# Kernel optimization log

Measured on AMD Instinct MI355X. Metric: run time of the kernel, lower is better.

## Reference

```python
import jax, jax.numpy as jnp
import numpy as np

N_HEADS = 12
LN_EPS = 1e-5


def _layernorm(x, g, b):
    mu = jnp.mean(x, axis=-1, keepdims=True)
    var = jnp.var(x, axis=-1, keepdims=True)
    return (x - mu) * jax.lax.rsqrt(var + LN_EPS) * g + b


def setup_inputs() -> dict:
    key = jax.random.key(0)
    ks = jax.random.split(key, 16)
    L, V, D, F, MAXS = 4, 32000, 768, 3072, 2048
    B, S = 2, 1024
    sd = 0.02
    inp = {
        'x': jax.random.randint(ks[0], (B, S), 0, V, dtype=jnp.int64),
        'tok_emb': jax.random.normal(ks[1], (V, D), jnp.float32) * sd,
        'pos_emb': jax.random.normal(ks[2], (MAXS, D), jnp.float32) * sd,
        'Wq': jax.random.normal(ks[3], (L, D, D), jnp.float32) * sd,
        'bq': jnp.zeros((L, D), jnp.float32),
        'Wk': jax.random.normal(ks[4], (L, D, D), jnp.float32) * sd,
        'bk': jnp.zeros((L, D), jnp.float32),
        'Wv': jax.random.normal(ks[5], (L, D, D), jnp.float32) * sd,
        'bv': jnp.zeros((L, D), jnp.float32),
        'Wo': jax.random.normal(ks[6], (L, D, D), jnp.float32) * sd,
        'bo': jnp.zeros((L, D), jnp.float32),
        'W1': jax.random.normal(ks[7], (L, F, D), jnp.float32) * sd,
        'b1': jnp.zeros((L, F), jnp.float32),
        'W2': jax.random.normal(ks[8], (L, D, F), jnp.float32) * sd,
        'b2': jnp.zeros((L, D), jnp.float32),
        'ln1_g': jnp.ones((L, D), jnp.float32),
        'ln1_b': jnp.zeros((L, D), jnp.float32),
        'ln2_g': jnp.ones((L, D), jnp.float32),
        'ln2_b': jnp.zeros((L, D), jnp.float32),
        'lnf_g': jnp.ones((D,), jnp.float32),
        'lnf_b': jnp.zeros((D,), jnp.float32),
    }
    return inp


def reference(x, tok_emb, pos_emb, Wq, bq, Wk, bk, Wv, bv, Wo, bo,
              W1, b1, W2, b2, ln1_g, ln1_b, ln2_g, ln2_b, lnf_g, lnf_b):
    B, S = x.shape
    D = tok_emb.shape[1]
    L = Wq.shape[0]
    H = N_HEADS
    dk = D // H
    scale = 1.0 / jnp.sqrt(jnp.float32(dk))

    h = tok_emb[x] + pos_emb[:S][None]  # [B,S,D]  (dropout p=0 -> identity)
    causal = jnp.tril(jnp.ones((S, S), bool))  # [S,S]

    def split_heads(t):  # [B,S,D] -> [B,H,S,dk]
        return t.reshape(B, S, H, dk).transpose(0, 2, 1, 3)

    for l in range(L):
        y = _layernorm(h, ln1_g[l], ln1_b[l])
        q = split_heads(y @ Wq[l].T + bq[l])
        k = split_heads(y @ Wk[l].T + bk[l])
        v = split_heads(y @ Wv[l].T + bv[l])
        scores = jnp.einsum('bhqd,bhkd->bhqk', q, k) * scale
        scores = jnp.where(causal, scores, -jnp.inf)
        attn = jax.nn.softmax(scores, axis=-1)
        ctx = jnp.einsum('bhqk,bhkd->bhqd', attn, v)
        ctx = ctx.transpose(0, 2, 1, 3).reshape(B, S, D)
        h = h + (ctx @ Wo[l].T + bo[l])
        y2 = _layernorm(h, ln2_g[l], ln2_b[l])
        ff = jax.nn.relu(y2 @ W1[l].T + b1[l]) @ W2[l].T + b2[l]
        h = h + ff

    h = _layernorm(h, lnf_g, lnf_b)
    logits = h @ tok_emb.T  # tied LM head, no bias
    return logits
```

## Files before the change

### kernel.cpp

```cpp
#include <hip/hip_runtime.h>
#include <hip/hip_bf16.h>

typedef __bf16 bf16_t;
typedef __bf16 bf16x8 __attribute__((ext_vector_type(8)));
typedef float floatx4 __attribute__((ext_vector_type(4)));

#define D_MODEL 768
#define N_HEADS 12
#define DK 64
#define SEQ 1024
#define BATCH 2
#define NROWS (BATCH * SEQ)
#define FFN 3072
#define VOCAB 32000
#define N_LAYERS 4
#define LN_EPS 1e-5f

__device__ __forceinline__ float block_reduce_256(float v, bool is_max, float* sb) {
#pragma unroll
    for (int off = 32; off > 0; off >>= 1) {
        float o = __shfl_down(v, off, 64);
        v = is_max ? fmaxf(v, o) : (v + o);
    }
    int lane = threadIdx.x & 63, wid = threadIdx.x >> 6;
    if (lane == 0) sb[wid] = v;
    __syncthreads();
    float r = is_max ? fmaxf(fmaxf(sb[0], sb[1]), fmaxf(sb[2], sb[3]))
                     : (sb[0] + sb[1]) + (sb[2] + sb[3]);
    __syncthreads();
    return r;
}

__global__ __launch_bounds__(256) void embed_kernel(const int* __restrict__ x,
                                                    const float* __restrict__ tok,
                                                    const float* __restrict__ pos,
                                                    float* __restrict__ h) {
    int row = blockIdx.x;
    int s = row & (SEQ - 1);
    int t = x[row];
    const float* te = tok + (size_t)t * D_MODEL;
    const float* pe = pos + (size_t)s * D_MODEL;
    float* out = h + (size_t)row * D_MODEL;
    int tid = threadIdx.x;
    out[tid]       = te[tid]       + pe[tid];
    out[tid + 256] = te[tid + 256] + pe[tid + 256];
    out[tid + 512] = te[tid + 512] + pe[tid + 512];
}

__global__ __launch_bounds__(256) void cvt_bf16_kernel(const float* __restrict__ src,
                                                       bf16_t* __restrict__ dst) {
    size_t i = ((size_t)blockIdx.x * 256 + threadIdx.x) * 8;
    const float4 a = *(const float4*)(src + i);
    const float4 b = *(const float4*)(src + i + 4);
    bf16x8 o;
    o[0] = (bf16_t)a.x; o[1] = (bf16_t)a.y; o[2] = (bf16_t)a.z; o[3] = (bf16_t)a.w;
    o[4] = (bf16_t)b.x; o[5] = (bf16_t)b.y; o[6] = (bf16_t)b.z; o[7] = (bf16_t)b.w;
    *(bf16x8*)(dst + i) = o;
}
static_assert((VOCAB * D_MODEL) % 2048 == 0, "cvt tiling");
static_assert((N_LAYERS * D_MODEL * D_MODEL) % 2048 == 0, "cvt tiling");
static_assert((N_LAYERS * FFN * D_MODEL) % 2048 == 0, "cvt tiling");

__global__ __launch_bounds__(256) void pack_qkvw_kernel(const float* __restrict__ Wq,
                                                        const float* __restrict__ Wk,
                                                        const float* __restrict__ Wv,
                                                        bf16_t* __restrict__ dst) {
    size_t e = ((size_t)blockIdx.x * 256 + threadIdx.x) * 8;
    const int PER_L = 3 * D_MODEL * D_MODEL;
    const int SEG   = D_MODEL * D_MODEL;
    int l   = (int)(e / PER_L);
    int rem = (int)(e - (size_t)l * PER_L);
    int n   = rem / D_MODEL;
    int c   = rem - n * D_MODEL;
    int seg = n / D_MODEL;
    int sr  = n - seg * D_MODEL;
    const float* src = (seg == 0 ? Wq : seg == 1 ? Wk : Wv) +
                       (size_t)l * SEG + (size_t)sr * D_MODEL + c;
    const float4 a = *(const float4*)src;
    const float4 b = *(const float4*)(src + 4);
    bf16x8 o;
    o[0] = (bf16_t)a.x; o[1] = (bf16_t)a.y; o[2] = (bf16_t)a.z; o[3] = (bf16_t)a.w;
    o[4] = (bf16_t)b.x; o[5] = (bf16_t)b.y; o[6] = (bf16_t)b.z; o[7] = (bf16_t)b.w;
    *(bf16x8*)(dst + e) = o;
}

__global__ __launch_bounds__(256) void pack_bias_kernel(const float* __restrict__ bq,
                                                        const float* __restrict__ bk,
                                                        const float* __restrict__ bv,
                                                        float* __restrict__ dst) {
    int i = blockIdx.x * 256 + threadIdx.x;
    int l = i / (3 * D_MODEL);
    int n = i - l * (3 * D_MODEL);
    int seg = n / D_MODEL;
    int sr  = n - seg * D_MODEL;
    dst[i] = (seg == 0 ? bq : seg == 1 ? bk : bv)[l * D_MODEL + sr];
}

__global__ __launch_bounds__(256) void ln_kernel(const float* __restrict__ h,
                                                 const float* __restrict__ g,
                                                 const float* __restrict__ b,
                                                 bf16_t* __restrict__ y) {
    __shared__ float sb[4];
    int row = blockIdx.x;
    const float* xr = h + (size_t)row * D_MODEL;
    int t = threadIdx.x;
    float v0 = xr[t], v1 = xr[t + 256], v2 = xr[t + 512];
    float s  = block_reduce_256(v0 + v1 + v2, false, sb);
    float s2 = block_reduce_256(v0 * v0 + v1 * v1 + v2 * v2, false, sb);
    float mu  = s * (1.0f / D_MODEL);
    float var = s2 * (1.0f / D_MODEL) - mu * mu;
    float inv = rsqrtf(var + LN_EPS);
    bf16_t* yr = y + (size_t)row * D_MODEL;
    yr[t]       = (bf16_t)((v0 - mu) * inv * g[t]       + b[t]);
    yr[t + 256] = (bf16_t)((v1 - mu) * inv * g[t + 256] + b[t + 256]);
    yr[t + 512] = (bf16_t)((v2 - mu) * inv * g[t + 512] + b[t + 512]);
}

template <typename OutT, bool RELU, bool HAS_BIAS, bool HAS_RES, bool MSWAP>
__global__ __launch_bounds__(256) void gemm_bt(const bf16_t* __restrict__ A,
                                               const float* __restrict__ W,
                                               const float* __restrict__ bias,
                                               const float* __restrict__ res,
                                               OutT* __restrict__ C,
                                               int M, int N, int K) {
    const int LDR = 40;
    __shared__ bf16_t As[64 * LDR];
    __shared__ bf16_t Bs[64 * LDR];
    const int m0 = (MSWAP ? blockIdx.x : blockIdx.y) * 64;
    const int n0 = (MSWAP ? blockIdx.y : blockIdx.x) * 64;
    const int tid  = threadIdx.x;
    const int wave = tid >> 6;
    const int lane = tid & 63;
    const int q    = lane >> 4;
    const int ln16 = lane & 15;

    floatx4 acc[4] = {{0.f, 0.f, 0.f, 0.f}, {0.f, 0.f, 0.f, 0.f},
                      {0.f, 0.f, 0.f, 0.f}, {0.f, 0.f, 0.f, 0.f}};

    const int srow = tid >> 2;
    const int scol = (tid & 3) * 8;
    const bf16_t* Aptr = A + (size_t)(m0 + srow) * K + scol;
    const float*  Wptr = W + (size_t)(n0 + srow) * K + scol;

    for (int k0 = 0; k0 < K; k0 += 32) {
        *(uint4*)(&As[srow * LDR + scol]) = *(const uint4*)(Aptr + k0);
        float4 w0 = *(const float4*)(Wptr + k0);
        float4 w1 = *(const float4*)(Wptr + k0 + 4);
        bf16x8 wb;
        wb[0] = (bf16_t)w0.x; wb[1] = (bf16_t)w0.y; wb[2] = (bf16_t)w0.z; wb[3] = (bf16_t)w0.w;
        wb[4] = (bf16_t)w1.x; wb[5] = (bf16_t)w1.y; wb[6] = (bf16_t)w1.z; wb[7] = (bf16_t)w1.w;
        *(bf16x8*)(&Bs[srow * LDR + scol]) = wb;
        __syncthreads();
        const bf16x8 a = *(const bf16x8*)(&As[(wave * 16 + ln16) * LDR + q * 8]);
#pragma unroll
        for (int nt = 0; nt < 4; nt++) {
            const bf16x8 b = *(const bf16x8*)(&Bs[(nt * 16 + ln16) * LDR + q * 8]);
            acc[nt] = __builtin_amdgcn_mfma_f32_16x16x32_bf16(a, b, acc[nt], 0, 0, 0);
        }
        __syncthreads();
    }

#pragma unroll
    for (int nt = 0; nt < 4; nt++) {
        const int n = n0 + nt * 16 + ln16;
        float bv = 0.f;
        if constexpr (HAS_BIAS) bv = bias[n];
#pragma unroll
        for (int r = 0; r < 4; r++) {
            const int m = m0 + wave * 16 + q * 4 + r;
            float v = acc[nt][r] + bv;
            if constexpr (RELU) v = fmaxf(v, 0.f);
            if constexpr (HAS_RES) v += res[(size_t)m * N + n];
            C[(size_t)m * N + n] = (OutT)v;
        }
    }
}

typedef __attribute__((address_space(3))) unsigned int lds_uint;
typedef const __attribute__((address_space(1))) unsigned int glb_uint;
__device__ __forceinline__ void gload16(const bf16_t* g, bf16_t* l) {
    __builtin_amdgcn_global_load_lds((glb_uint*)g, (lds_uint*)l, 16, 0, 0);
}

template <typename OutT, bool RELU, bool HAS_BIAS, bool HAS_RES, bool NTS, int TN>
__global__ __launch_bounds__(256) void gemm128(const bf16_t* __restrict__ A,
                                               const bf16_t* __restrict__ W,
                                               const float* __restrict__ bias,
                                               const float* __restrict__ res,
                                               OutT* __restrict__ C,
                                               int M, int N, int K) {
    constexpr int NFR = TN / 32;
    __shared__ __align__(16) bf16_t As[128 * 32];
    __shared__ __align__(16) bf16_t Bs[TN * 32];
    const int m0 = blockIdx.x * 128;
    const int n0 = blockIdx.y * TN;
    const int tid  = threadIdx.x;
    const int wave = tid >> 6;
    const int lane = tid & 63;
    const int q    = lane >> 4;
    const int ln16 = lane & 15;
    const int wr   = wave >> 1;
    const int wc   = wave & 1;

    floatx4 acc[4][NFR];
#pragma unroll
    for (int i = 0; i < 4; i++)
#pragma unroll
        for (int j = 0; j < NFR; j++) acc[i][j] = (floatx4){0.f, 0.f, 0.f, 0.f};

    const int srow = lane >> 2;
    const int scol = (lane & 3) * 8;
    const bf16_t* Ag = A + (size_t)(m0 + wave * 32 + srow) * K + scol;
    const bf16_t* Wg = W + (size_t)(n0 + wave * (TN / 4) + srow) * K + scol;
    bf16_t* As0 = &As[wave * 1024];
    bf16_t* Bs0 = &Bs[wave * (TN / 4) * 32];

    for (int k0 = 0; k0 < K; k0 += 32) {
        gload16(Ag + k0, As0);
        gload16(Ag + (size_t)16 * K + k0, As0 + 512);
        gload16(Wg + k0, Bs0);
        if constexpr (TN == 128) gload16(Wg + (size_t)16 * K + k0, Bs0 + 512);
        __syncthreads();
        bf16x8 af[4], bfg[NFR];
#pragma unroll
        for (int mt = 0; mt < 4; mt++)
            af[mt] = *(const bf16x8*)&As[(wr * 64 + mt * 16 + ln16) * 32 + q * 8];
#pragma unroll
        for (int nt = 0; nt < NFR; nt++)
            bfg[nt] = *(const bf16x8*)&Bs[(wc * (TN / 2) + nt * 16 + ln16) * 32 + q * 8];
#pragma unroll
        for (int mt = 0; mt < 4; mt++)
#pragma unroll
            for (int nt = 0; nt < NFR; nt++)
                acc[mt][nt] = __builtin_amdgcn_mfma_f32_16x16x32_bf16(af[mt], bfg[nt], acc[mt][nt], 0, 0, 0);
        __syncthreads();
    }

#pragma unroll
    for (int mt = 0; mt < 4; mt++)
#pragma unroll
        for (int nt = 0; nt < NFR; nt++) {
            const int n = n0 + wc * (TN / 2) + nt * 16 + ln16;
            float bv = 0.f;
            if constexpr (HAS_BIAS) bv = bias[n];
#pragma unroll
            for (int r = 0; r < 4; r++) {
                const int m = m0 + wr * 64 + mt * 16 + q * 4 + r;
                float v = acc[mt][nt][r] + bv;
                if constexpr (RELU) v = fmaxf(v, 0.f);
                if constexpr (HAS_RES) v += res[(size_t)m * N + n];
                if constexpr (NTS) {
                    __builtin_nontemporal_store((OutT)v, &C[(size_t)m * N + n]);
                } else {
                    C[(size_t)m * N + n] = (OutT)v;
                }
            }
        }
}

__global__ __launch_bounds__(256) void attn_kernel(const bf16_t* __restrict__ Q,
                                                   const bf16_t* __restrict__ K,
                                                   const bf16_t* __restrict__ V,
                                                   bf16_t* __restrict__ ctx,
                                                   int ld) {
    __shared__ bf16_t smem[12288];
    bf16_t* Qs  = smem;
    bf16_t* Ks  = smem + 4096;
    bf16_t* Vts = smem + 8192;
    bf16_t* Ps  = smem;

    const int qt  = blockIdx.x;
    const int bh  = blockIdx.y;
    const int b   = bh / N_HEADS;
    const int hh  = bh - b * N_HEADS;
    const int tid  = threadIdx.x;
    const int wave = tid >> 6;
    const int lane = tid & 63;
    const int quad = lane >> 4;
    const int ln16 = lane & 15;
    const int q0   = qt * 64;
    const size_t base = (size_t)(b * SEQ) * ld + hh * DK;

    const int r0 = tid >> 3;
    const int cg = tid & 7;

    {
        const bf16_t* src = Q + base + (size_t)q0 * ld;
        *(uint4*)&Qs[r0 * 64 + cg * 8]        = *(const uint4*)(src + (size_t)r0 * ld + cg * 8);
        *(uint4*)&Qs[(r0 + 32) * 64 + cg * 8] = *(const uint4*)(src + (size_t)(r0 + 32) * ld + cg * 8);
    }
    __syncthreads();
    const bf16x8 aq0 = *(const bf16x8*)&Qs[(wave * 16 + ln16) * 64 + quad * 8];
    const bf16x8 aq1 = *(const bf16x8*)&Qs[(wave * 16 + ln16) * 64 + 32 + quad * 8];

    float m_run[4] = {-1e30f, -1e30f, -1e30f, -1e30f};
    float l_run[4] = {0.f, 0.f, 0.f, 0.f};
    floatx4 o[4] = {{0.f, 0.f, 0.f, 0.f}, {0.f, 0.f, 0.f, 0.f},
                    {0.f, 0.f, 0.f, 0.f}, {0.f, 0.f, 0.f, 0.f}};
    const float scale = 0.125f;

    for (int j0 = 0; j0 <= q0; j0 += 64) {
        __syncthreads();
        const bf16_t* ksrc = K + base + (size_t)j0 * ld;
        const bf16_t* vsrc = V + base + (size_t)j0 * ld;
#pragma unroll
        for (int half = 0; half < 2; half++) {
            const int j = r0 + half * 32;
            *(uint4*)&Ks[j * 64 + cg * 8] = *(const uint4*)(ksrc + (size_t)j * ld + cg * 8);
            const bf16x8 vv = *(const bf16x8*)(vsrc + (size_t)j * ld + cg * 8);
#pragma unroll
            for (int i = 0; i < 8; i++) {
                const int d = cg * 8 + i;
                Vts[d * 64 + (((j >> 3) ^ cg) << 3) + (j & 7)] = vv[i];
            }
        }
        __syncthreads();

        floatx4 s[4];
#pragma unroll
        for (int nt = 0; nt < 4; nt++) {
            const bf16x8 bk0 = *(const bf16x8*)&Ks[(nt * 16 + ln16) * 64 + quad * 8];
            const bf16x8 bk1 = *(const bf16x8*)&Ks[(nt * 16 + ln16) * 64 + 32 + quad * 8];
            floatx4 z = {0.f, 0.f, 0.f, 0.f};
            z = __builtin_amdgcn_mfma_f32_16x16x32_bf16(aq0, bk0, z, 0, 0, 0);
            z = __builtin_amdgcn_mfma_f32_16x16x32_bf16(aq1, bk1, z, 0, 0, 0);
            s[nt] = z;
        }
        const bool diag = (j0 == q0);
#pragma unroll
        for (int nt = 0; nt < 4; nt++)
#pragma unroll
            for (int r = 0; r < 4; r++) {
                float v = s[nt][r] * scale;
                if (diag && (nt * 16 + ln16 > wave * 16 + quad * 4 + r)) v = -1e30f;
                s[nt][r] = v;
            }

        float alpha[4];
#pragma unroll
        for (int r = 0; r < 4; r++) {
            float v = fmaxf(fmaxf(s[0][r], s[1][r]), fmaxf(s[2][r], s[3][r]));
#pragma unroll
            for (int off = 1; off < 16; off <<= 1) v = fmaxf(v, __shfl_xor(v, off, 64));
            const float m_new = fmaxf(m_run[r], v);
            alpha[r] = __expf(m_run[r] - m_new);
            m_run[r] = m_new;
        }
        float rsum[4] = {0.f, 0.f, 0.f, 0.f};
#pragma unroll
        for (int nt = 0; nt < 4; nt++)
#pragma unroll
            for (int r = 0; r < 4; r++) {
                const float p = __expf(s[nt][r] - m_run[r]);
                s[nt][r] = p;
                rsum[r] += p;
            }
#pragma unroll
        for (int r = 0; r < 4; r++) {
            float v = rsum[r];
#pragma unroll
            for (int off = 1; off < 16; off <<= 1) v += __shfl_xor(v, off, 64);
            l_run[r] = l_run[r] * alpha[r] + v;
        }
#pragma unroll
        for (int nt = 0; nt < 4; nt++)
#pragma unroll
            for (int r = 0; r < 4; r++) o[nt][r] *= alpha[r];

        bf16_t* Pw = Ps + wave * 1024;
#pragma unroll
        for (int nt = 0; nt < 4; nt++)
#pragma unroll
            for (int r = 0; r < 4; r++) {
                const int rr = quad * 4 + r;
                Pw[rr * 64 + (((nt * 2 + (ln16 >> 3)) ^ (rr & 7)) << 3) + (ln16 & 7)] = (bf16_t)s[nt][r];
            }
        const bf16x8 ap0 = *(const bf16x8*)&Pw[ln16 * 64 + ((quad ^ (ln16 & 7)) << 3)];
        const bf16x8 ap1 = *(const bf16x8*)&Pw[ln16 * 64 + (((quad + 4) ^ (ln16 & 7)) << 3)];

#pragma unroll
        for (int nt = 0; nt < 4; nt++) {
            const int d  = nt * 16 + ln16;
            const int dd = (nt * 2 + (ln16 >> 3)) & 7;
            const bf16x8 bv0 = *(const bf16x8*)&Vts[d * 64 + ((quad ^ dd) << 3)];
            const bf16x8 bv1 = *(const bf16x8*)&Vts[d * 64 + (((quad + 4) ^ dd) << 3)];
            o[nt] = __builtin_amdgcn_mfma_f32_16x16x32_bf16(ap0, bv0, o[nt], 0, 0, 0);
            o[nt] = __builtin_amdgcn_mfma_f32_16x16x32_bf16(ap1, bv1, o[nt], 0, 0, 0);
        }
    }

#pragma unroll
    for (int r = 0; r < 4; r++) {
        const float inv = 1.0f / l_run[r];
        const int m = q0 + wave * 16 + quad * 4 + r;
#pragma unroll
        for (int nt = 0; nt < 4; nt++) {
            ctx[(size_t)(b * SEQ + m) * D_MODEL + hh * DK + nt * 16 + ln16] = (bf16_t)(o[nt][r] * inv);
        }
    }
}

extern "C" void kernel_launch(void* const* d_in, const int* in_sizes, int n_in,
                              void* d_out, int out_size, void* d_ws, size_t ws_size,
                              hipStream_t stream) {
    const int*   x    = (const int*)d_in[0];
    const float* tok  = (const float*)d_in[1];
    const float* pos  = (const float*)d_in[2];
    const float* Wq   = (const float*)d_in[3];
    const float* bq   = (const float*)d_in[4];
    const float* Wk   = (const float*)d_in[5];
    const float* bk   = (const float*)d_in[6];
    const float* Wv   = (const float*)d_in[7];
    const float* bv   = (const float*)d_in[8];
    const float* Wo   = (const float*)d_in[9];
    const float* bo   = (const float*)d_in[10];
    const float* W1   = (const float*)d_in[11];
    const float* b1   = (const float*)d_in[12];
    const float* W2   = (const float*)d_in[13];
    const float* b2   = (const float*)d_in[14];
    const float* ln1g = (const float*)d_in[15];
    const float* ln1b = (const float*)d_in[16];
    const float* ln2g = (const float*)d_in[17];
    const float* ln2b = (const float*)d_in[18];
    const float* lnfg = (const float*)d_in[19];
    const float* lnfb = (const float*)d_in[20];

    char* ws = (char*)d_ws;
    const size_t OFF_H    = 0;
    const size_t OFF_Y    = 6291456;
    const size_t OFF_QKV  = 9437184;
    const size_t OFF_CTX  = 18874368;
    const size_t OFF_FF   = OFF_QKV;
    const size_t OFF_TOKB = 22020096;
    const size_t OFF_WB   = 71172096;
    const size_t OFF_BQKV = 127795200;
    const size_t END_ALL  = 127832064;
    const size_t END_TOKB = OFF_WB;

    const bool big_ws  = ws_size >= END_TOKB;
    const bool big2_ws = ws_size >= END_ALL;

    float*  h    = (float*)(ws + OFF_H);
    bf16_t* y    = (bf16_t*)(ws + OFF_Y);
    bf16_t* qkv  = (bf16_t*)(ws + OFF_QKV);
    bf16_t* qb   = qkv;
    bf16_t* kb   = qkv + 2048 * 768;
    bf16_t* vbuf = qkv + 2 * 2048 * 768;
    bf16_t* ctx  = (bf16_t*)(ws + OFF_CTX);
    bf16_t* ff   = (bf16_t*)(ws + OFF_FF);
    bf16_t* tokb = (bf16_t*)(ws + OFF_TOKB);
    bf16_t* wb   = (bf16_t*)(ws + OFF_WB);
    bf16_t* wqkvb = wb;
    bf16_t* wob   = wb + 7077888;
    bf16_t* w1b   = wb + 9437184;
    bf16_t* w2b   = wb + 18874368;
    float*  bqkv  = (float*)(ws + OFF_BQKV);
    float*  outp  = (float*)d_out;

    embed_kernel<<<NROWS, 256, 0, stream>>>(x, tok, pos, h);

    if (big_ws) {
        cvt_bf16_kernel<<<(VOCAB * D_MODEL) / 2048, 256, 0, stream>>>(tok, tokb);
    }
    if (big2_ws) {
        pack_qkvw_kernel<<<(N_LAYERS * 3 * D_MODEL * D_MODEL) / 2048, 256, 0, stream>>>(Wq, Wk, Wv, wqkvb);
        cvt_bf16_kernel<<<(N_LAYERS * D_MODEL * D_MODEL) / 2048, 256, 0, stream>>>(Wo, wob);
        cvt_bf16_kernel<<<(N_LAYERS * FFN * D_MODEL) / 2048, 256, 0, stream>>>(W1, w1b);
        cvt_bf16_kernel<<<(N_LAYERS * FFN * D_MODEL) / 2048, 256, 0, stream>>>(W2, w2b);
        pack_bias_kernel<<<(N_LAYERS * 3 * D_MODEL) / 256, 256, 0, stream>>>(bq, bk, bv, bqkv);
    }

    const dim3 g768(D_MODEL / 64, NROWS / 64);
    const dim3 gffn(FFN / 64, NROWS / 64);
    const dim3 gattn(SEQ / 64, BATCH * N_HEADS);

    for (int l = 0; l < N_LAYERS; l++) {
        const float* Wq_l = Wq + (size_t)l * D_MODEL * D_MODEL;
        const float* Wk_l = Wk + (size_t)l * D_MODEL * D_MODEL;
        const float* Wv_l = Wv + (size_t)l * D_MODEL * D_MODEL;
        const float* Wo_l = Wo + (size_t)l * D_MODEL * D_MODEL;
        const float* W1_l = W1 + (size_t)l * FFN * D_MODEL;
        const float* W2_l = W2 + (size_t)l * D_MODEL * FFN;

        ln_kernel<<<NROWS, 256, 0, stream>>>(h, ln1g + l * D_MODEL, ln1b + l * D_MODEL, y);

        if (big2_ws) {
            gemm128<bf16_t, false, true, false, false, 128>
                <<<dim3(NROWS / 128, (3 * D_MODEL) / 128), 256, 0, stream>>>(
                y, wqkvb + (size_t)l * 3 * D_MODEL * D_MODEL, bqkv + l * 3 * D_MODEL,
                nullptr, qkv, NROWS, 3 * D_MODEL, D_MODEL);

            attn_kernel<<<gattn, 256, 0, stream>>>(qkv, qkv + D_MODEL, qkv + 2 * D_MODEL, ctx, 3 * D_MODEL);

            gemm128<float, false, true, true, false, 64>
                <<<dim3(NROWS / 128, D_MODEL / 64), 256, 0, stream>>>(
                ctx, wob + (size_t)l * D_MODEL * D_MODEL, bo + l * D_MODEL,
                h, h, NROWS, D_MODEL, D_MODEL);

            ln_kernel<<<NROWS, 256, 0, stream>>>(h, ln2g + l * D_MODEL, ln2b + l * D_MODEL, y);

            gemm128<bf16_t, true, true, false, false, 128>
                <<<dim3(NROWS / 128, FFN / 128), 256, 0, stream>>>(
                y, w1b + (size_t)l * FFN * D_MODEL, b1 + l * FFN,
                nullptr, ff, NROWS, FFN, D_MODEL);

            gemm128<float, false, true, true, false, 64>
                <<<dim3(NROWS / 128, D_MODEL / 64), 256, 0, stream>>>(
                ff, w2b + (size_t)l * D_MODEL * FFN, b2 + l * D_MODEL,
                h, h, NROWS, D_MODEL, FFN);
        } else {
            gemm_bt<bf16_t, false, true, false, false><<<g768, 256, 0, stream>>>(
                y, Wq_l, bq + l * D_MODEL, nullptr, qb, NROWS, D_MODEL, D_MODEL);
            gemm_bt<bf16_t, false, true, false, false><<<g768, 256, 0, stream>>>(
                y, Wk_l, bk + l * D_MODEL, nullptr, kb, NROWS, D_MODEL, D_MODEL);
            gemm_bt<bf16_t, false, true, false, false><<<g768, 256, 0, stream>>>(
                y, Wv_l, bv + l * D_MODEL, nullptr, vbuf, NROWS, D_MODEL, D_MODEL);

            attn_kernel<<<gattn, 256, 0, stream>>>(qb, kb, vbuf, ctx, D_MODEL);

            gemm_bt<float, false, true, true, false><<<g768, 256, 0, stream>>>(
                ctx, Wo_l, bo + l * D_MODEL, h, h, NROWS, D_MODEL, D_MODEL);

            ln_kernel<<<NROWS, 256, 0, stream>>>(h, ln2g + l * D_MODEL, ln2b + l * D_MODEL, y);

            gemm_bt<bf16_t, true, true, false, false><<<gffn, 256, 0, stream>>>(
                y, W1_l, b1 + l * FFN, nullptr, ff, NROWS, FFN, D_MODEL);

            gemm_bt<float, false, true, true, false><<<g768, 256, 0, stream>>>(
                ff, W2_l, b2 + l * D_MODEL, h, h, NROWS, D_MODEL, FFN);
        }
    }

    ln_kernel<<<NROWS, 256, 0, stream>>>(h, lnfg, lnfb, y);

    if (big_ws) {
        gemm128<float, false, false, false, true, 128>
            <<<dim3(NROWS / 128, VOCAB / 128), 256, 0, stream>>>(
            y, tokb, nullptr, nullptr, outp, NROWS, VOCAB, D_MODEL);
    } else {
        gemm_bt<float, false, false, false, true><<<dim3(NROWS / 64, VOCAB / 64), 256, 0, stream>>>(
            y, tok, nullptr, nullptr, outp, NROWS, VOCAB, D_MODEL);
    }
}
```

Measured before the change: 1.255 ms.

## Deepen GEMM K-tile to 64 with XOR-swizzled LDS and XCD-aware block remap

The 128xTN GEMM now stages 64-wide K slices per iteration instead of 32, halving the number of barrier pairs per K loop and issuing two MFMA k-steps per sync. LDS rows are written and read with an XOR swizzle on the 16-byte chunk index to avoid bank conflicts at the new 128-byte row stride. A template flag optionally remaps block IDs so consecutive blocks are spread across the 8 XCDs for better L2 locality, and it replaces the nontemporal-store option. The cost is doubled LDS use, which may lower occupancy, and the last-layer logits output no longer uses nontemporal stores.

```diff
diff --git a/kernel.cpp b/kernel.cpp
--- a/kernel.cpp
+++ b/kernel.cpp
@@ -182,7 +182,7 @@
     __builtin_amdgcn_global_load_lds((glb_uint*)g, (lds_uint*)l, 16, 0, 0);
 }
 
-template <typename OutT, bool RELU, bool HAS_BIAS, bool HAS_RES, bool NTS, int TN>
+template <typename OutT, bool RELU, bool HAS_BIAS, bool HAS_RES, bool XSWZ, int TN>
 __global__ __launch_bounds__(256) void gemm128(const bf16_t* __restrict__ A,
                                                const bf16_t* __restrict__ W,
                                                const float* __restrict__ bias,
@@ -190,10 +190,22 @@
                                                OutT* __restrict__ C,
                                                int M, int N, int K) {
     constexpr int NFR = TN / 32;
-    __shared__ __align__(16) bf16_t As[128 * 32];
-    __shared__ __align__(16) bf16_t Bs[TN * 32];
-    const int m0 = blockIdx.x * 128;
-    const int n0 = blockIdx.y * TN;
+    __shared__ __align__(16) bf16_t As[128 * 64];
+    __shared__ __align__(16) bf16_t Bs[TN * 64];
+
+    int mb, nb;
+    if constexpr (XSWZ) {
+        const int nwg = gridDim.x * gridDim.y;
+        const int lid = blockIdx.x + blockIdx.y * gridDim.x;
+        if ((nwg & 7) == 0) {
+            const int swz = (lid & 7) * (nwg >> 3) + (lid >> 3);
+            mb = swz % gridDim.x;
+            nb = swz / gridDim.x;
+        } else { mb = blockIdx.x; nb = blockIdx.y; }
+    } else { mb = blockIdx.x; nb = blockIdx.y; }
+
+    const int m0 = mb * 128;
+    const int n0 = nb * TN;
     const int tid  = threadIdx.x;
     const int wave = tid >> 6;
     const int lane = tid & 63;
@@ -208,31 +220,41 @@
 #pragma unroll
         for (int j = 0; j < NFR; j++) acc[i][j] = (floatx4){0.f, 0.f, 0.f, 0.f};
 
-    const int srow = lane >> 2;
-    const int scol = (lane & 3) * 8;
+    const int srow = lane >> 3;
+    const int scol = ((lane & 7) ^ srow) * 8;
     const bf16_t* Ag = A + (size_t)(m0 + wave * 32 + srow) * K + scol;
     const bf16_t* Wg = W + (size_t)(n0 + wave * (TN / 4) + srow) * K + scol;
-    bf16_t* As0 = &As[wave * 1024];
-    bf16_t* Bs0 = &Bs[wave * (TN / 4) * 32];
-
-    for (int k0 = 0; k0 < K; k0 += 32) {
-        gload16(Ag + k0, As0);
-        gload16(Ag + (size_t)16 * K + k0, As0 + 512);
-        gload16(Wg + k0, Bs0);
-        if constexpr (TN == 128) gload16(Wg + (size_t)16 * K + k0, Bs0 + 512);
+    bf16_t* As0 = &As[(wave * 32) * 64];
+    bf16_t* Bs0 = &Bs[(wave * (TN / 4)) * 64];
+
+    const int ps = ln16 & 7;
+
+    for (int k0 = 0; k0 < K; k0 += 64) {
+#pragma unroll
+        for (int i = 0; i < 4; i++)
+            gload16(Ag + (size_t)(i * 8) * K + k0, As0 + (i * 8) * 64);
+#pragma unroll
+        for (int i = 0; i < NFR; i++)
+            gload16(Wg + (size_t)(i * 8) * K + k0, Bs0 + (i * 8) * 64);
         __syncthreads();
-        bf16x8 af[4], bfg[NFR];
-#pragma unroll
-        for (int mt = 0; mt < 4; mt++)
-            af[mt] = *(const bf16x8*)&As[(wr * 64 + mt * 16 + ln16) * 32 + q * 8];
-#pragma unroll
-        for (int nt = 0; nt < NFR; nt++)
-            bfg[nt] = *(const bf16x8*)&Bs[(wc * (TN / 2) + nt * 16 + ln16) * 32 + q * 8];
-#pragma unroll
-        for (int mt = 0; mt < 4; mt++)
+
+        bf16x8 af[4][2], bfg[NFR][2];
+#pragma unroll
+        for (int kk = 0; kk < 2; kk++) {
+#pragma unroll
+            for (int mt = 0; mt < 4; mt++)
+                af[mt][kk] = *(const bf16x8*)&As[(wr * 64 + mt * 16 + ln16) * 64 + (((kk * 4 + q) ^ ps) << 3)];
 #pragma unroll
             for (int nt = 0; nt < NFR; nt++)
-                acc[mt][nt] = __builtin_amdgcn_mfma_f32_16x16x32_bf16(af[mt], bfg[nt], acc[mt][nt], 0, 0, 0);
+                bfg[nt][kk] = *(const bf16x8*)&Bs[(wc * (TN / 2) + nt * 16 + ln16) * 64 + (((kk * 4 + q) ^ ps) << 3)];
+        }
+#pragma unroll
+        for (int kk = 0; kk < 2; kk++)
+#pragma unroll
+            for (int mt = 0; mt < 4; mt++)
+#pragma unroll
+                for (int nt = 0; nt < NFR; nt++)
+                    acc[mt][nt] = __builtin_amdgcn_mfma_f32_16x16x32_bf16(af[mt][kk], bfg[nt][kk], acc[mt][nt], 0, 0, 0);
         __syncthreads();
     }
 
@@ -249,11 +271,7 @@
                 float v = acc[mt][nt][r] + bv;
                 if constexpr (RELU) v = fmaxf(v, 0.f);
                 if constexpr (HAS_RES) v += res[(size_t)m * N + n];
-                if constexpr (NTS) {
-                    __builtin_nontemporal_store((OutT)v, &C[(size_t)m * N + n]);
-                } else {
-                    C[(size_t)m * N + n] = (OutT)v;
-                }
+                C[(size_t)m * N + n] = (OutT)v;
             }
         }
 }
```

Result: faster. 1.218 ms (-2.9%).
